# Kernel tuning notes

Hardware: AMD Instinct MI355X
Metric: run time of the kernel (lower is better)

## Reference

```python
import jax, jax.numpy as jnp
import numpy as np

N_USER, N_ITEM, N_ENT, N_REL, D = 100000, 50000, 200000, 32, 64
N_EDGE, NNZ = 500000, 2000000
N_HOPS, N_GCN, RES_LAMBDA = 2, 2, 0.5
MIN_NORM = 1e-15
BALL_EPS = 1e-3  # Poincare ball (c=1) boundary clip, standard fp32 value


def _sqnorm(x):
    return jnp.sum(x * x, axis=-1, keepdims=True)


def _norm(x):
    return jnp.maximum(jnp.sqrt(_sqnorm(x)), MIN_NORM)


def project(x):
    # clip points to the open unit ball
    n = _norm(x)
    maxn = 1.0 - BALL_EPS
    return jnp.where(n > maxn, x / n * maxn, x)


def expmap0(u):
    # exp map at origin, c=1: tanh(||u||) * u/||u||
    n = _norm(u)
    return jnp.tanh(n) * u / n


def mobius_add(x, y):
    x2, y2 = _sqnorm(x), _sqnorm(y)
    xy = jnp.sum(x * y, axis=-1, keepdims=True)
    num = (1.0 + 2.0 * xy + y2) * x + (1.0 - x2) * y
    den = 1.0 + 2.0 * xy + x2 * y2
    return num / jnp.maximum(den, MIN_NORM)


def expmap(u, p):
    # exp map at base point p of tangent vector u
    n = _norm(u)
    lam = 2.0 / jnp.maximum(1.0 - _sqnorm(p), MIN_NORM)
    return mobius_add(p, jnp.tanh(0.5 * lam * n) * u / n)


def logmap(x, p):
    # log map at base point p of point x
    sub = mobius_add(-p, x)
    n = _norm(sub)
    lam = 2.0 / jnp.maximum(1.0 - _sqnorm(p), MIN_NORM)
    return (2.0 / lam) * jnp.arctanh(jnp.minimum(n, 1.0 - 1e-5)) * sub / n


def l2norm(x):
    # F.normalize(x, dim=-1), eps=1e-12
    return x / jnp.maximum(jnp.linalg.norm(x, axis=-1, keepdims=True), 1e-12)


def rgat_agg(ent, rel, head, tail, rtype):
    he, te, re = ent[head], ent[tail], rel[rtype]  # [E, D] gathers
    ricci = l2norm(te + re)
    hh = expmap0(he)
    ht = expmap(te, hh)
    hr = expmap(re, hh)
    res = project(mobius_add(ht, hr))
    res = logmap(res, hh) + ricci * 1e-7
    res = jax.nn.relu(res)
    sums = jax.ops.segment_sum(res, head, num_segments=N_ENT)
    cnt = jax.ops.segment_sum(jnp.ones((head.shape[0], 1), res.dtype), head, num_segments=N_ENT)
    return sums / jnp.maximum(cnt, 1.0)  # scatter_mean


def setup_inputs() -> dict:
    key = jax.random.key(0)
    ks = jax.random.split(key, 9)
    return {
        "uEmbeds": jax.random.normal(ks[0], (N_USER, D), jnp.float32) * 0.02,
        "eEmbeds": jax.random.normal(ks[1], (N_ENT, D), jnp.float32) * 0.02,
        "rEmbeds": jax.random.normal(ks[2], (N_REL, D), jnp.float32) * 0.02,
        "adj_val": jax.random.uniform(ks[8], (NNZ,), jnp.float32),
        "edge_head": jax.random.randint(ks[3], (N_EDGE,), 0, N_ENT),
        "edge_tail": jax.random.randint(ks[4], (N_EDGE,), 0, N_ENT),
        "edge_type": jax.random.randint(ks[5], (N_EDGE,), 1, N_REL),
        "adj_row": jax.random.randint(ks[6], (NNZ,), 0, N_USER + N_ITEM),
        "adj_col": jax.random.randint(ks[7], (NNZ,), 0, N_USER + N_ITEM),
    }


def reference(uEmbeds, eEmbeds, rEmbeds, adj_val, edge_head, edge_tail, edge_type, adj_row, adj_col):
    rtype = edge_type - 1
    ent_res = eEmbeds
    ent = eEmbeds
    for _ in range(N_HOPS):  # RGAT hops (mess_dropout=False for determinism)
        ent = rgat_agg(ent, rEmbeds, edge_head, edge_tail, rtype)
        ent = l2norm(ent)
        ent_res = RES_LAMBDA * ent_res + ent
    # concat users with first n_items entity embeddings
    embeds = jnp.concatenate([uEmbeds, ent_res[:N_ITEM]], axis=0)  # [user+item, D]
    total = embeds
    cur = embeds
    for _ in range(N_GCN):  # GCN layers: spmm(adj, embeds) in COO form
        cur = jax.ops.segment_sum(adj_val[:, None] * cur[adj_col], adj_row,
                                  num_segments=N_USER + N_ITEM)
        total = total + cur
    # original returns (total[:N_USER], total[N_USER:]); we return the concat
    return total
```

## Files before the change

### kernel.cpp

```cpp
#include <hip/hip_runtime.h>
#include <math.h>

#define D 64
#define MIN_NORM 1e-15f
#define NBINS 64
#define MAXBKT 1024
#define L1_TILE 4096
#define WCAP_A 3840
#define WCAP_E 1024

#define RCP(x)  __builtin_amdgcn_rcpf(x)
#define RSQ(x)  __builtin_amdgcn_rsqf(x)

template <int CTRL>
__device__ __forceinline__ float dpp_sum_step(float v) {
    int iv = __builtin_bit_cast(int, v);
    int sh = __builtin_amdgcn_update_dpp(0, iv, CTRL, 0xf, 0xf, true);
    return v + __builtin_bit_cast(float, sh);
}
#define DPP_XOR1  0xB1
#define DPP_XOR2  0x4E
#define DPP_HMIR  0x141
#define DPP_MIR   0x140

__device__ __forceinline__ float row16_sum(float v) {
    v = dpp_sum_step<DPP_XOR1>(v);
    v = dpp_sum_step<DPP_XOR2>(v);
    v = dpp_sum_step<DPP_HMIR>(v);
    v = dpp_sum_step<DPP_MIR>(v);
    return v;
}


__device__ __forceinline__ float fast_tanh_pos(float x) {
    float t = __expf(-2.0f * x);
    return (1.0f - t) * RCP(1.0f + t);
}

__device__ __forceinline__ float fast_atanh(float x) {
    return 0.5f * __logf((1.0f + x) * RCP(1.0f - x));
}


__global__ void rel_prep_kernel(const float* __restrict__ rel,
                                float* __restrict__ rtab, int n_rel)
{
    int r = threadIdx.x;
    if (r >= n_rel) return;
    float s = 0.0f;
    for (int d = 0; d < D; ++d) { float v = rel[r * D + d]; s += v * v; }
    float re2g = fmaxf(s, 1e-30f);
    float rn  = RSQ(re2g);
    float nre = re2g * rn;
    float a   = fast_tanh_pos(1.0f);
    float rm2 = RCP(fmaxf(1.0f - a * a, MIN_NORM));
    rtab[r]       = s;
    rtab[64 + r]  = rn;
    rtab[128 + r] = nre;
    rtab[192 + r] = fast_tanh_pos(nre * rm2) * rn;
}


template <int HOP>
__global__ __launch_bounds__(256) void rgat_head_kernel(
    const float* __restrict__ ent, const float* __restrict__ rel,
    const int* __restrict__ erow_ptr, const int2* __restrict__ pair_e,
    const int* __restrict__ headperm,
    const float* __restrict__ prev_res,
    const float* __restrict__ rtab, float* __restrict__ te2tab,
    float* __restrict__ ent_out, float* __restrict__ res_out,
    int n_ent)
{
    int g = blockIdx.x * 16 + (threadIdx.x >> 4);
    if (g >= n_ent) return;
    int sub = threadIdx.x & 15;
    int h = headperm[g];

    const float* hp = ent + (size_t)h * D + sub;
    float hex = hp[0], hey = hp[16], hez = hp[32], hew = hp[48];

    float HE2, a, HH2, mterm, rmterm, bconst;
    if (HOP == 1) {
        HE2 = row16_sum(hex*hex + hey*hey + hez*hez + hew*hew);
        float HE2g = fmaxf(HE2, 1e-30f);
        float rNhe = RSQ(HE2g);
        float Nhe  = HE2g * rNhe;
        a = fast_tanh_pos(Nhe) * rNhe;
        HH2 = a * a * HE2;
        mterm = fmaxf(1.0f - HH2, MIN_NORM);
        rmterm = RCP(mterm);
        bconst = 0.0f;
    } else {
        HE2 = 1.0f;
        a = fast_tanh_pos(1.0f);
        HH2 = a * a;
        mterm = 1.0f - HH2;
        rmterm = RCP(mterm);
        bconst = fast_tanh_pos(rmterm);
    }

    float ax = 0.0f, ay = 0.0f, az = 0.0f, aw = 0.0f;
    int s = erow_ptr[h];
    int e = erow_ptr[h + 1];

    for (int i = s; i < e; ++i) {
        int2 pe = pair_e[i];
        int tcol = pe.x;
        int rr = pe.y - 1;
        const float* tp = ent + (size_t)tcol * D + sub;
        const float* rp = rel + (size_t)rr * D + sub;
        float tex = tp[0], tey = tp[16], tez = tp[32], tew = tp[48];
        float rex = rp[0], rey = rp[16], rez = rp[32], rew = rp[48];

        float HT = row16_sum(hex*tex + hey*tey + hez*tez + hew*tew);
        float HR = row16_sum(hex*rex + hey*rey + hez*rez + hew*rew);
        float TR = row16_sum(tex*rex + tey*rey + tez*rez + tew*rew);

        float TE2;
        if (HOP == 1) TE2 = row16_sum(tex*tex + tey*tey + tez*tez + tew*tew);
        else          TE2 = te2tab[tcol];

        float RE2  = rtab[rr];
        float rNre = rtab[64 + rr];

        float ricci_k = 1e-7f * RSQ(fmaxf(TE2 + 2.0f * TR + RE2, 1e-24f));

        float b, c;
        if (HOP == 1) {
            float TE2g = fmaxf(TE2, 1e-30f);
            float rNte = RSQ(TE2g);
            b = fast_tanh_pos(TE2g * rNte * rmterm) * rNte;
            c = fast_tanh_pos(rtab[128 + rr] * rmterm) * rNre;
        } else {
            b = bconst;
            c = rtab[192 + rr];
        }

        float y2t = b * b * TE2, xyt = a * b * HT;
        float A1 = 1.0f + 2.0f * xyt + y2t, B1 = 1.0f - HH2;
        float r_d1 = RCP(fmaxf(1.0f + 2.0f * xyt + HH2 * y2t, MIN_NORM));
        float p1 = A1 * a * r_d1, q1 = B1 * b * r_d1;
        float HT2 = fmaxf((A1*A1*HH2 + 2.0f*A1*B1*xyt + B1*B1*y2t) * r_d1 * r_d1, 0.0f);

        float y2r = c * c * RE2, xyr = a * c * HR;
        float A2 = 1.0f + 2.0f * xyr + y2r, B2 = 1.0f - HH2;
        float r_d2 = RCP(fmaxf(1.0f + 2.0f * xyr + HH2 * y2r, MIN_NORM));
        float p2 = A2 * a * r_d2, q2 = B2 * c * r_d2;
        float HR2 = fmaxf((A2*A2*HH2 + 2.0f*A2*B2*xyr + B2*B2*y2r) * r_d2 * r_d2, 0.0f);

        float xy3 = p1*p2*HE2 + p1*q2*HR + q1*p2*HT + q1*q2*TR;
        float A3 = 1.0f + 2.0f * xy3 + HR2, B3 = 1.0f - HT2;
        float r_d3 = RCP(fmaxf(1.0f + 2.0f * xy3 + HT2 * HR2, MIN_NORM));
        float al = (A3 * p1 + B3 * p2) * r_d3;
        float be = A3 * q1 * r_d3;
        float ga = B3 * q2 * r_d3;
        float R2 = fmaxf((A3*A3*HT2 + 2.0f*A3*B3*xy3 + B3*B3*HR2) * r_d3 * r_d3, 0.0f);

        float R2g = fmaxf(R2, 1e-30f);
        float rNr = RSQ(R2g);
        float Nr  = R2g * rNr;
        const float maxn = 1.0f - 1e-3f;
        if (Nr > maxn) {
            float sc = maxn * rNr;
            al *= sc; be *= sc; ga *= sc;
            R2 = maxn * maxn;
        }

        float dhr = a * (al * HE2 + be * HT + ga * HR);
        float xy4 = -dhr;
        float A4 = 1.0f + 2.0f * xy4 + R2, B4 = 1.0f - HH2;
        float r_d4 = RCP(fmaxf(1.0f + 2.0f * xy4 + HH2 * R2, MIN_NORM));
        float sh = (-A4 * a + B4 * al) * r_d4;
        float st = B4 * be * r_d4;
        float sr = B4 * ga * r_d4;
        float SUB2 = fmaxf((A4*A4*HH2 + 2.0f*A4*B4*xy4 + B4*B4*R2) * r_d4 * r_d4, 0.0f);

        float SUB2g = fmaxf(SUB2, 1e-30f);
        float rNsub = RSQ(SUB2g);
        float Nsub  = SUB2g * rNsub;
        float k = mterm * fast_atanh(fminf(Nsub, 1.0f - 1e-5f)) * rNsub;

        float kh = k * sh;
        float kt = k * st + ricci_k;
        float kr = k * sr + ricci_k;

        ax += fmaxf(kh*hex + kt*tex + kr*rex, 0.0f);
        ay += fmaxf(kh*hey + kt*tey + kr*rey, 0.0f);
        az += fmaxf(kh*hez + kt*tez + kr*rez, 0.0f);
        aw += fmaxf(kh*hew + kt*tew + kr*rew, 0.0f);
    }

    float rc = RCP(fmaxf((float)(e - s), 1.0f));
    float mx = ax*rc, my = ay*rc, mz = az*rc, mw = aw*rc;
    float M2 = row16_sum(mx*mx + my*my + mz*mz + mw*mw);
    float rn = RSQ(fmaxf(M2, 1e-24f));
    mx *= rn; my *= rn; mz *= rn; mw *= rn;

    if (HOP == 1) {
        float* ep = ent_out + (size_t)h * D + sub;
        ep[0] = mx; ep[16] = my; ep[32] = mz; ep[48] = mw;
        if (sub == 0) te2tab[h] = (M2 > 1e-24f) ? 1.0f : 0.0f;
    }
    const float* pp = prev_res + (size_t)h * D + sub;
    float* rp2 = res_out + (size_t)h * D + sub;
    rp2[0]  = 0.5f*pp[0]  + mx;
    rp2[16] = 0.5f*pp[16] + my;
    rp2[32] = 0.5f*pp[32] + mz;
    rp2[48] = 0.5f*pp[48] + mw;
}


__global__ __launch_bounds__(256) void deg_hist_kernel(
    const int* __restrict__ erow_ptr, int* __restrict__ dbins, int n_heads)
{
    __shared__ int lbin[NBINS];
    int tid = threadIdx.x;
    if (tid < NBINS) lbin[tid] = 0;
    __syncthreads();
    int h = blockIdx.x * 256 + tid;
    if (h < n_heads) {
        int d = min(erow_ptr[h + 1] - erow_ptr[h], NBINS - 1);
        atomicAdd(&lbin[d], 1);
    }
    __syncthreads();
    if (tid < NBINS) { int c = lbin[tid]; if (c) atomicAdd(&dbins[tid], c); }
}

__global__ void deg_scan_kernel(const int* __restrict__ dbins, int* __restrict__ bin_cursor)
{
    int tid = threadIdx.x;
    int v = dbins[tid];
    int incl = v;
#pragma unroll
    for (int off = 1; off < 64; off <<= 1) {
        int u = __shfl_up(incl, off, 64);
        if (tid >= off) incl += u;
    }
    int T = __shfl(incl, 63, 64);
    bin_cursor[tid] = T - incl;
}

__global__ __launch_bounds__(256) void deg_scatter_kernel(
    const int* __restrict__ erow_ptr, int* __restrict__ bin_cursor,
    int* __restrict__ headperm, int n_heads)
{
    __shared__ int lbin[NBINS];
    __shared__ int lbase[NBINS];
    int tid = threadIdx.x;
    if (tid < NBINS) lbin[tid] = 0;
    __syncthreads();
    int h = blockIdx.x * 256 + tid;
    int b = 0, lpos = 0;
    bool act = (h < n_heads);
    if (act) {
        b = min(erow_ptr[h + 1] - erow_ptr[h], NBINS - 1);
        lpos = atomicAdd(&lbin[b], 1);
    }
    __syncthreads();
    if (tid < NBINS) { int c = lbin[tid]; lbase[tid] = c ? atomicAdd(&bin_cursor[tid], c) : 0; }
    __syncthreads();
    if (act) headperm[lbase[b] + lpos] = h;
}


__global__ void concat_init_kernel(const float4* __restrict__ u,
                                   const float4* __restrict__ res,
                                   float4* __restrict__ bufA,
                                   int user4, int total4)
{
    int i = blockIdx.x * blockDim.x + threadIdx.x;
    if (i >= total4) return;
    float4 v = (i < user4) ? u[i] : res[i - user4];
    bufA[i] = v;
}


__global__ __launch_bounds__(256) void bucket_l1_kernel(
    const int* __restrict__ key, const int* __restrict__ col,
    const int* __restrict__ vbits,
    int* __restrict__ bktcur, int2* __restrict__ bkt,
    int n, int nbkt, int cap)
{
    __shared__ int lcnt[MAXBKT];
    __shared__ int lofs[MAXBKT];
    __shared__ int gofs[MAXBKT];
    __shared__ int lpos[MAXBKT];
    __shared__ int wsum[4];
    __shared__ int2 lent[L1_TILE];
    __shared__ unsigned short lbkt[L1_TILE];

    int tid  = threadIdx.x;
    int lane = tid & 63;
    int wave = tid >> 6;
    int base = blockIdx.x * L1_TILE;
    int cnt_total = min(n - base, L1_TILE);

    for (int b = tid; b < MAXBKT; b += 256) lcnt[b] = 0;
    __syncthreads();

#pragma unroll
    for (int k = 0; k < L1_TILE / 256; ++k) {
        int i = base + k * 256 + tid;
        if (i < n) atomicAdd(&lcnt[key[i] >> 8], 1);
    }
    __syncthreads();

    int b0 = tid * 4;
    int c0 = lcnt[b0], c1 = lcnt[b0 + 1], c2 = lcnt[b0 + 2], c3 = lcnt[b0 + 3];
    int tot = c0 + c1 + c2 + c3;
    int incl = tot;
#pragma unroll
    for (int off = 1; off < 64; off <<= 1) {
        int u = __shfl_up(incl, off, 64);
        if (lane >= off) incl += u;
    }
    if (lane == 63) wsum[wave] = incl;
    __syncthreads();
    int woff = 0;
    for (int w = 0; w < wave; ++w) woff += wsum[w];
    int excl = woff + incl - tot;
    lofs[b0]     = excl;                lpos[b0]     = excl;
    lofs[b0 + 1] = excl + c0;           lpos[b0 + 1] = excl + c0;
    lofs[b0 + 2] = excl + c0 + c1;      lpos[b0 + 2] = excl + c0 + c1;
    lofs[b0 + 3] = excl + c0 + c1 + c2; lpos[b0 + 3] = excl + c0 + c1 + c2;
    for (int b = tid; b < nbkt; b += 256) {
        int c = lcnt[b];
        gofs[b] = c ? atomicAdd(&bktcur[b], c) : 0;
    }
    __syncthreads();

#pragma unroll
    for (int k = 0; k < L1_TILE / 256; ++k) {
        int i = base + k * 256 + tid;
        if (i < n) {
            int r = key[i];
            int b = r >> 8;
            int p = atomicAdd(&lpos[b], 1);
            lent[p] = make_int2((col[i] << 8) | (r & 255), vbits[i]);
            lbkt[p] = (unsigned short)b;
        }
    }
    __syncthreads();

    for (int j = tid; j < cnt_total; j += 256) {
        int b = lbkt[j];
        int off = gofs[b] + (j - lofs[b]);
        if (off < cap) bkt[(size_t)b * cap + off] = lent[j];
    }
}

__global__ __launch_bounds__(256) void win_scan_kernel(
    const int* __restrict__ wincnt, int* __restrict__ winbase, int nwin, int cap)
{
    __shared__ int wsum[4];
    int tid = threadIdx.x, lane = tid & 63, wave = tid >> 6;
    int b = tid * 4;
    int c0 = (b + 0 < nwin) ? min(wincnt[b + 0], cap) : 0;
    int c1 = (b + 1 < nwin) ? min(wincnt[b + 1], cap) : 0;
    int c2 = (b + 2 < nwin) ? min(wincnt[b + 2], cap) : 0;
    int c3 = (b + 3 < nwin) ? min(wincnt[b + 3], cap) : 0;
    int tot = c0 + c1 + c2 + c3;
    int incl = tot;
#pragma unroll
    for (int off = 1; off < 64; off <<= 1) {
        int u = __shfl_up(incl, off, 64);
        if (lane >= off) incl += u;
    }
    if (lane == 63) wsum[wave] = incl;
    __syncthreads();
    int woff = 0;
    for (int w = 0; w < wave; ++w) woff += wsum[w];
    int excl = woff + incl - tot;
    if (b + 0 < nwin) winbase[b + 0] = excl;
    if (b + 1 < nwin) winbase[b + 1] = excl + c0;
    if (b + 2 < nwin) winbase[b + 2] = excl + c0 + c1;
    if (b + 3 < nwin) winbase[b + 3] = excl + c0 + c1 + c2;
}

__global__ __launch_bounds__(256) void place_l2b_kernel(
    const int* __restrict__ wincnt, const int* __restrict__ winbase,
    const int2* __restrict__ bkt,
    int2* __restrict__ pair, int* __restrict__ row_ptr,
    int n_keys, int nwin, int cap)
{
    __shared__ int rcnt[256];
    __shared__ int rofs[256];
    __shared__ int wsum[4];
    int w = blockIdx.x;
    int tid = threadIdx.x;
    int lane = tid & 63, wave = tid >> 6;
    int rbase = w << 8;
    int cnt = min(wincnt[w], cap);
    int base = winbase[w];
    const int2* seg = bkt + (size_t)w * cap;

    rcnt[tid] = 0;
    __syncthreads();
    for (int i = tid; i < cnt; i += 256)
        atomicAdd(&rcnt[bkt[(size_t)w * cap + i].x & 255], 1);
    __syncthreads();

    int v = rcnt[tid];
    int incl = v;
#pragma unroll
    for (int off = 1; off < 64; off <<= 1) {
        int u = __shfl_up(incl, off, 64);
        if (lane >= off) incl += u;
    }
    if (lane == 63) wsum[wave] = incl;
    __syncthreads();
    int woff = 0;
    for (int i = 0; i < wave; ++i) woff += wsum[i];
    int excl = woff + incl - v;
    rofs[tid] = excl;
    int r = rbase + tid;
    if (r < n_keys) row_ptr[r] = base + excl;
    if (w == nwin - 1 && tid == 255) row_ptr[n_keys] = base + excl + v;
    __syncthreads();

    for (int i = tid; i < cnt; i += 256) {
        int2 q = seg[i];
        int pos = base + atomicAdd(&rofs[q.x & 255], 1);
        pair[pos] = make_int2(q.x >> 8, q.y);
    }
}


__device__ __forceinline__ float spmm_row_gather(
    const int2* __restrict__ pair, const float* __restrict__ cur,
    int s, int e, int lane)
{
    int cnt = e - s;
    if (cnt <= 0) return 0.0f;
    int nv = min(cnt, 64);
    int2 q = pair[s + min(lane, nv - 1)];

    float acc0 = 0.0f, acc1 = 0.0f, acc2 = 0.0f, acc3 = 0.0f;
    float acc4 = 0.0f, acc5 = 0.0f, acc6 = 0.0f, acc7 = 0.0f;

    for (int base = 0; base < nv; base += 8) {
        int c0 = __builtin_amdgcn_readlane(q.x, base + 0);
        int c1 = __builtin_amdgcn_readlane(q.x, base + 1);
        int c2 = __builtin_amdgcn_readlane(q.x, base + 2);
        int c3 = __builtin_amdgcn_readlane(q.x, base + 3);
        int c4 = __builtin_amdgcn_readlane(q.x, base + 4);
        int c5 = __builtin_amdgcn_readlane(q.x, base + 5);
        int c6 = __builtin_amdgcn_readlane(q.x, base + 6);
        int c7 = __builtin_amdgcn_readlane(q.x, base + 7);
        float x0 = cur[(size_t)c0 * D + lane];
        float x1 = cur[(size_t)c1 * D + lane];
        float x2 = cur[(size_t)c2 * D + lane];
        float x3 = cur[(size_t)c3 * D + lane];
        float x4 = cur[(size_t)c4 * D + lane];
        float x5 = cur[(size_t)c5 * D + lane];
        float x6 = cur[(size_t)c6 * D + lane];
        float x7 = cur[(size_t)c7 * D + lane];
        float v0 = (base + 0 < nv) ? __int_as_float(__builtin_amdgcn_readlane(q.y, base + 0)) : 0.0f;
        float v1 = (base + 1 < nv) ? __int_as_float(__builtin_amdgcn_readlane(q.y, base + 1)) : 0.0f;
        float v2 = (base + 2 < nv) ? __int_as_float(__builtin_amdgcn_readlane(q.y, base + 2)) : 0.0f;
        float v3 = (base + 3 < nv) ? __int_as_float(__builtin_amdgcn_readlane(q.y, base + 3)) : 0.0f;
        float v4 = (base + 4 < nv) ? __int_as_float(__builtin_amdgcn_readlane(q.y, base + 4)) : 0.0f;
        float v5 = (base + 5 < nv) ? __int_as_float(__builtin_amdgcn_readlane(q.y, base + 5)) : 0.0f;
        float v6 = (base + 6 < nv) ? __int_as_float(__builtin_amdgcn_readlane(q.y, base + 6)) : 0.0f;
        float v7 = (base + 7 < nv) ? __int_as_float(__builtin_amdgcn_readlane(q.y, base + 7)) : 0.0f;
        acc0 = fmaf(v0, x0, acc0);
        acc1 = fmaf(v1, x1, acc1);
        acc2 = fmaf(v2, x2, acc2);
        acc3 = fmaf(v3, x3, acc3);
        acc4 = fmaf(v4, x4, acc4);
        acc5 = fmaf(v5, x5, acc5);
        acc6 = fmaf(v6, x6, acc6);
        acc7 = fmaf(v7, x7, acc7);
    }
    for (int i = s + 64; i < e; ++i) {
        int2 p = pair[i];
        acc0 = fmaf(__int_as_float(p.y), cur[(size_t)p.x * D + lane], acc0);
    }
    return ((acc0 + acc1) + (acc2 + acc3)) + ((acc4 + acc5) + (acc6 + acc7));
}

__global__ __launch_bounds__(256) void spmm_l1_kernel(
    const int* __restrict__ row_ptr, const int2* __restrict__ pair,
    const float* __restrict__ cur, float* __restrict__ nxt, int n_rows)
{
    int row = blockIdx.x * 4 + (threadIdx.x >> 6);
    if (row >= n_rows) return;
    int lane = threadIdx.x & 63;
    int s = row_ptr[row];
    int e = row_ptr[row + 1];
    float acc = spmm_row_gather(pair, cur, s, e, lane);
    nxt[(size_t)row * D + lane] = acc;
}

__global__ __launch_bounds__(256) void spmm_l2_kernel(
    const int* __restrict__ row_ptr, const int2* __restrict__ pair,
    const float* __restrict__ cur1, const float* __restrict__ embeds,
    float* __restrict__ out, int n_rows)
{
    int row = blockIdx.x * 4 + (threadIdx.x >> 6);
    if (row >= n_rows) return;
    int lane = threadIdx.x & 63;
    int s = row_ptr[row];
    int e = row_ptr[row + 1];
    float acc = spmm_row_gather(pair, cur1, s, e, lane);
    size_t idx = (size_t)row * D + lane;
    float emb = __builtin_nontemporal_load(embeds + idx);
    float c1  = cur1[idx];
    __builtin_nontemporal_store(emb + c1 + acc, out + idx);
}


extern "C" void kernel_launch(void* const* d_in, const int* in_sizes, int n_in,
                              void* d_out, int out_size, void* d_ws, size_t ws_size,
                              hipStream_t stream)
{
    const float* uE      = (const float*)d_in[0];
    const float* eE      = (const float*)d_in[1];
    const float* rE      = (const float*)d_in[2];
    const float* adj_val = (const float*)d_in[3];
    const int*   e_head  = (const int*)d_in[4];
    const int*   e_tail  = (const int*)d_in[5];
    const int*   e_type  = (const int*)d_in[6];
    const int*   a_row   = (const int*)d_in[7];
    const int*   a_col   = (const int*)d_in[8];

    const int n_user  = in_sizes[0] / D;
    const int n_ent   = in_sizes[1] / D;
    const int n_rel   = in_sizes[2] / D;
    const int nnz     = in_sizes[3];
    const int n_edges = in_sizes[4];
    const int n_rows  = out_size / D;

    float* ws = (float*)d_ws;
    const size_t entElems = (size_t)n_ent * D;
    float* ent1    = ws;
    float* ent_res = ws + entElems;
    int*   r3      = (int*)(ws + 2 * entElems);

    int2* ebkt = (int2*)ent_res;
    int2* abkt = (int2*)ent_res;

    const int nep = n_ent + 4;
    int*  erow_ptr = r3;
    int2* pair_e   = (int2*)(erow_ptr + nep);
    int*  headperm = (int*)(pair_e + n_edges);
    int*  dbins    = headperm + n_ent;
    int*  bincur   = dbins + NBINS;
    int*  ewincur  = bincur + NBINS;
    int*  ewinbase = ewincur + MAXBKT;
    float* te2tab  = (float*)(ewinbase + MAXBKT);
    float* rtab    = te2tab + n_ent;

    int*  row_ptr  = r3;
    int2* pair     = (int2*)(row_ptr + (n_rows + 4));
    int*  awincur  = (int*)(pair + nnz);
    int*  awinbase = awincur + MAXBKT;

    float* out = (float*)d_out;

    const int nbkt_e = (n_ent + 255) / 256;
    hipMemsetAsync(dbins, 0, (2 * NBINS + MAXBKT) * sizeof(int), stream);
    rel_prep_kernel<<<1, 64, 0, stream>>>(rE, rtab, n_rel);
    bucket_l1_kernel<<<(n_edges + L1_TILE - 1) / L1_TILE, 256, 0, stream>>>(
        e_head, e_tail, (const int*)e_type, ewincur, ebkt, n_edges, nbkt_e, WCAP_E);
    win_scan_kernel<<<1, 256, 0, stream>>>(ewincur, ewinbase, nbkt_e, WCAP_E);
    place_l2b_kernel<<<nbkt_e, 256, 0, stream>>>(ewincur, ewinbase, ebkt,
                                                 pair_e, erow_ptr, n_ent, nbkt_e, WCAP_E);
    deg_hist_kernel<<<(n_ent + 255) / 256, 256, 0, stream>>>(erow_ptr, dbins, n_ent);
    deg_scan_kernel<<<1, 64, 0, stream>>>(dbins, bincur);
    deg_scatter_kernel<<<(n_ent + 255) / 256, 256, 0, stream>>>(erow_ptr, bincur,
                                                                headperm, n_ent);

    const int head_blocks = (n_ent + 15) / 16;
    rgat_head_kernel<1><<<head_blocks, 256, 0, stream>>>(eE, rE, erow_ptr, pair_e,
                                                         headperm, eE, rtab, te2tab,
                                                         ent1, ent_res, n_ent);
    rgat_head_kernel<2><<<head_blocks, 256, 0, stream>>>(ent1, rE, erow_ptr, pair_e,
                                                         headperm, ent_res, rtab, te2tab,
                                                         ent1, ent_res, n_ent);

    float* bufA = ent1;
    float* bufB = ent_res;

    const int total4 = n_rows * (D / 4);
    const int user4  = n_user * (D / 4);

    concat_init_kernel<<<(total4 + 255) / 256, 256, 0, stream>>>(
        (const float4*)uE, (const float4*)ent_res, (float4*)bufA, user4, total4);

    const int nbkt_a = (n_rows + 255) / 256;
    hipMemsetAsync(awincur, 0, (size_t)MAXBKT * sizeof(int), stream);
    bucket_l1_kernel<<<(nnz + L1_TILE - 1) / L1_TILE, 256, 0, stream>>>(
        a_row, a_col, (const int*)adj_val, awincur, abkt, nnz, nbkt_a, WCAP_A);
    win_scan_kernel<<<1, 256, 0, stream>>>(awincur, awinbase, nbkt_a, WCAP_A);
    place_l2b_kernel<<<nbkt_a, 256, 0, stream>>>(awincur, awinbase, abkt,
                                                 pair, row_ptr, n_rows, nbkt_a, WCAP_A);

    const int row_blocks = (n_rows + 3) / 4;
    spmm_l1_kernel<<<row_blocks, 256, 0, stream>>>(row_ptr, pair, bufA, bufB, n_rows);
    spmm_l2_kernel<<<row_blocks, 256, 0, stream>>>(row_ptr, pair, bufB, bufA, out, n_rows);
}
```

Before: 555.9 us.

## Fuse scan and histogram kernels into producers via last-block-done counters

Removes the two hipMemsetAsync calls and four small kernels (win_scan twice, deg_hist, deg_scan). Zeroing moves into rel_prep and concat_init, the window scan runs in the last finishing block of bucket_l1, and the degree histogram and scan fold into place_l2b via an atomic done counter. The aim is to cut launch and serialization gaps between tiny kernels, at the cost of a threadfence and atomic per block and a serial tail in the last block. place_l2b also reads through the existing seg pointer instead of reindexing bkt.

```diff
diff --git a/kernel.cpp b/kernel.cpp
--- a/kernel.cpp
+++ b/kernel.cpp
@@ -42,10 +42,13 @@
 }
 
 
-__global__ void rel_prep_kernel(const float* __restrict__ rel,
-                                float* __restrict__ rtab, int n_rel)
-{
-    int r = threadIdx.x;
+__global__ __launch_bounds__(256) void rel_prep_kernel(
+    const float* __restrict__ rel, float* __restrict__ rtab,
+    int* __restrict__ zbase, int nzero, int n_rel)
+{
+    int tid = threadIdx.x;
+    for (int i = tid; i < nzero; i += 256) zbase[i] = 0;
+    int r = tid;
     if (r >= n_rel) return;
     float s = 0.0f;
     for (int d = 0; d < D; ++d) { float v = rel[r * D + d]; s += v * v; }
@@ -210,36 +213,6 @@
 }
 
 
-__global__ __launch_bounds__(256) void deg_hist_kernel(
-    const int* __restrict__ erow_ptr, int* __restrict__ dbins, int n_heads)
-{
-    __shared__ int lbin[NBINS];
-    int tid = threadIdx.x;
-    if (tid < NBINS) lbin[tid] = 0;
-    __syncthreads();
-    int h = blockIdx.x * 256 + tid;
-    if (h < n_heads) {
-        int d = min(erow_ptr[h + 1] - erow_ptr[h], NBINS - 1);
-        atomicAdd(&lbin[d], 1);
-    }
-    __syncthreads();
-    if (tid < NBINS) { int c = lbin[tid]; if (c) atomicAdd(&dbins[tid], c); }
-}
-
-__global__ void deg_scan_kernel(const int* __restrict__ dbins, int* __restrict__ bin_cursor)
-{
-    int tid = threadIdx.x;
-    int v = dbins[tid];
-    int incl = v;
-#pragma unroll
-    for (int off = 1; off < 64; off <<= 1) {
-        int u = __shfl_up(incl, off, 64);
-        if (tid >= off) incl += u;
-    }
-    int T = __shfl(incl, 63, 64);
-    bin_cursor[tid] = T - incl;
-}
-
 __global__ __launch_bounds__(256) void deg_scatter_kernel(
     const int* __restrict__ erow_ptr, int* __restrict__ bin_cursor,
     int* __restrict__ headperm, int n_heads)
@@ -266,9 +239,11 @@
 __global__ void concat_init_kernel(const float4* __restrict__ u,
                                    const float4* __restrict__ res,
                                    float4* __restrict__ bufA,
+                                   int* __restrict__ azero, int nzero,
                                    int user4, int total4)
 {
     int i = blockIdx.x * blockDim.x + threadIdx.x;
+    if (i < nzero) azero[i] = 0;
     if (i >= total4) return;
     float4 v = (i < user4) ? u[i] : res[i - user4];
     bufA[i] = v;
@@ -279,6 +254,7 @@
     const int* __restrict__ key, const int* __restrict__ col,
     const int* __restrict__ vbits,
     int* __restrict__ bktcur, int2* __restrict__ bkt,
+    int* __restrict__ done_ctr, int* __restrict__ winbase,
     int n, int nbkt, int cap)
 {
     __shared__ int lcnt[MAXBKT];
@@ -286,6 +262,7 @@
     __shared__ int gofs[MAXBKT];
     __shared__ int lpos[MAXBKT];
     __shared__ int wsum[4];
+    __shared__ int lastf;
     __shared__ int2 lent[L1_TILE];
     __shared__ unsigned short lbkt[L1_TILE];
 
@@ -347,40 +324,46 @@
         int off = gofs[b] + (j - lofs[b]);
         if (off < cap) bkt[(size_t)b * cap + off] = lent[j];
     }
-}
-
-__global__ __launch_bounds__(256) void win_scan_kernel(
-    const int* __restrict__ wincnt, int* __restrict__ winbase, int nwin, int cap)
-{
-    __shared__ int wsum[4];
-    int tid = threadIdx.x, lane = tid & 63, wave = tid >> 6;
-    int b = tid * 4;
-    int c0 = (b + 0 < nwin) ? min(wincnt[b + 0], cap) : 0;
-    int c1 = (b + 1 < nwin) ? min(wincnt[b + 1], cap) : 0;
-    int c2 = (b + 2 < nwin) ? min(wincnt[b + 2], cap) : 0;
-    int c3 = (b + 3 < nwin) ? min(wincnt[b + 3], cap) : 0;
-    int tot = c0 + c1 + c2 + c3;
-    int incl = tot;
+
+    __syncthreads();
+    if (tid == 0) {
+        __threadfence();
+        lastf = (atomicAdd(done_ctr, 1) == (int)gridDim.x - 1);
+    }
+    __syncthreads();
+    if (lastf) {
+        int sb = tid * 4;
+        int s0 = (sb + 0 < nbkt) ? min(atomicAdd(&bktcur[sb + 0], 0), cap) : 0;
+        int s1 = (sb + 1 < nbkt) ? min(atomicAdd(&bktcur[sb + 1], 0), cap) : 0;
+        int s2 = (sb + 2 < nbkt) ? min(atomicAdd(&bktcur[sb + 2], 0), cap) : 0;
+        int s3 = (sb + 3 < nbkt) ? min(atomicAdd(&bktcur[sb + 3], 0), cap) : 0;
+        int st = s0 + s1 + s2 + s3;
+        int sincl = st;
 #pragma unroll
-    for (int off = 1; off < 64; off <<= 1) {
-        int u = __shfl_up(incl, off, 64);
-        if (lane >= off) incl += u;
-    }
-    if (lane == 63) wsum[wave] = incl;
-    __syncthreads();
-    int woff = 0;
-    for (int w = 0; w < wave; ++w) woff += wsum[w];
-    int excl = woff + incl - tot;
-    if (b + 0 < nwin) winbase[b + 0] = excl;
-    if (b + 1 < nwin) winbase[b + 1] = excl + c0;
-    if (b + 2 < nwin) winbase[b + 2] = excl + c0 + c1;
-    if (b + 3 < nwin) winbase[b + 3] = excl + c0 + c1 + c2;
-}
-
+        for (int off = 1; off < 64; off <<= 1) {
+            int u = __shfl_up(sincl, off, 64);
+            if (lane >= off) sincl += u;
+        }
+        if (lane == 63) wsum[wave] = sincl;
+        __syncthreads();
+        int swoff = 0;
+        for (int w = 0; w < wave; ++w) swoff += wsum[w];
+        int sexcl = swoff + sincl - st;
+        if (sb + 0 < nbkt) winbase[sb + 0] = sexcl;
+        if (sb + 1 < nbkt) winbase[sb + 1] = sexcl + s0;
+        if (sb + 2 < nbkt) winbase[sb + 2] = sexcl + s0 + s1;
+        if (sb + 3 < nbkt) winbase[sb + 3] = sexcl + s0 + s1 + s2;
+    }
+}
+
+
+template <int DEG>
 __global__ __launch_bounds__(256) void place_l2b_kernel(
     const int* __restrict__ wincnt, const int* __restrict__ winbase,
     const int2* __restrict__ bkt,
     int2* __restrict__ pair, int* __restrict__ row_ptr,
+    int* __restrict__ dbins, int* __restrict__ bin_cursor,
+    int* __restrict__ done_ctr,
     int n_keys, int nwin, int cap)
 {
     __shared__ int rcnt[256];
@@ -397,7 +380,7 @@
     rcnt[tid] = 0;
     __syncthreads();
     for (int i = tid; i < cnt; i += 256)
-        atomicAdd(&rcnt[bkt[(size_t)w * cap + i].x & 255], 1);
+        atomicAdd(&rcnt[seg[i].x & 255], 1);
     __syncthreads();
 
     int v = rcnt[tid];
@@ -422,6 +405,33 @@
         int2 q = seg[i];
         int pos = base + atomicAdd(&rofs[q.x & 255], 1);
         pair[pos] = make_int2(q.x >> 8, q.y);
+    }
+
+    if (DEG) {
+        __shared__ int lbin[NBINS];
+        __shared__ int lastf;
+        if (tid < NBINS) lbin[tid] = 0;
+        __syncthreads();
+        if (r < n_keys) atomicAdd(&lbin[min(v, NBINS - 1)], 1);
+        __syncthreads();
+        if (tid < NBINS) { int cb = lbin[tid]; if (cb) atomicAdd(&dbins[tid], cb); }
+        __syncthreads();
+        if (tid == 0) {
+            __threadfence();
+            lastf = (atomicAdd(done_ctr, 1) == (int)gridDim.x - 1);
+        }
+        __syncthreads();
+        if (lastf && tid < 64) {
+            int dv = atomicAdd(&dbins[tid], 0);
+            int dincl = dv;
+#pragma unroll
+            for (int off = 1; off < 64; off <<= 1) {
+                int u = __shfl_up(dincl, off, 64);
+                if (tid >= off) dincl += u;
+            }
+            int T = __shfl(dincl, 63, 64);
+            bin_cursor[tid] = T - dincl;
+        }
     }
 }
 
@@ -547,27 +557,30 @@
     int*  dbins    = headperm + n_ent;
     int*  bincur   = dbins + NBINS;
     int*  ewincur  = bincur + NBINS;
-    int*  ewinbase = ewincur + MAXBKT;
+    int*  ectrs    = ewincur + MAXBKT;
+    int*  ewinbase = ectrs + 4;
     float* te2tab  = (float*)(ewinbase + MAXBKT);
     float* rtab    = te2tab + n_ent;
+    const int nzero_e = NBINS + NBINS + MAXBKT + 4;
 
     int*  row_ptr  = r3;
     int2* pair     = (int2*)(row_ptr + (n_rows + 4));
     int*  awincur  = (int*)(pair + nnz);
-    int*  awinbase = awincur + MAXBKT;
+    int*  actrs    = awincur + MAXBKT;
+    int*  awinbase = actrs + 4;
+    const int nzero_a = MAXBKT + 4;
 
     float* out = (float*)d_out;
 
     const int nbkt_e = (n_ent + 255) / 256;
-    hipMemsetAsync(dbins, 0, (2 * NBINS + MAXBKT) * sizeof(int), stream);
-    rel_prep_kernel<<<1, 64, 0, stream>>>(rE, rtab, n_rel);
+    rel_prep_kernel<<<1, 256, 0, stream>>>(rE, rtab, dbins, nzero_e, n_rel);
     bucket_l1_kernel<<<(n_edges + L1_TILE - 1) / L1_TILE, 256, 0, stream>>>(
-        e_head, e_tail, (const int*)e_type, ewincur, ebkt, n_edges, nbkt_e, WCAP_E);
-    win_scan_kernel<<<1, 256, 0, stream>>>(ewincur, ewinbase, nbkt_e, WCAP_E);
-    place_l2b_kernel<<<nbkt_e, 256, 0, stream>>>(ewincur, ewinbase, ebkt,
-                                                 pair_e, erow_ptr, n_ent, nbkt_e, WCAP_E);
-    deg_hist_kernel<<<(n_ent + 255) / 256, 256, 0, stream>>>(erow_ptr, dbins, n_ent);
-    deg_scan_kernel<<<1, 64, 0, stream>>>(dbins, bincur);
+        e_head, e_tail, (const int*)e_type, ewincur, ebkt, &ectrs[0], ewinbase,
+        n_edges, nbkt_e, WCAP_E);
+    place_l2b_kernel<1><<<nbkt_e, 256, 0, stream>>>(ewincur, ewinbase, ebkt,
+                                                    pair_e, erow_ptr,
+                                                    dbins, bincur, &ectrs[1],
+                                                    n_ent, nbkt_e, WCAP_E);
     deg_scatter_kernel<<<(n_ent + 255) / 256, 256, 0, stream>>>(erow_ptr, bincur,
                                                                 headperm, n_ent);
 
@@ -586,15 +599,17 @@
     const int user4  = n_user * (D / 4);
 
     concat_init_kernel<<<(total4 + 255) / 256, 256, 0, stream>>>(
-        (const float4*)uE, (const float4*)ent_res, (float4*)bufA, user4, total4);
+        (const float4*)uE, (const float4*)ent_res, (float4*)bufA,
+        awincur, nzero_a, user4, total4);
 
     const int nbkt_a = (n_rows + 255) / 256;
-    hipMemsetAsync(awincur, 0, (size_t)MAXBKT * sizeof(int), stream);
     bucket_l1_kernel<<<(nnz + L1_TILE - 1) / L1_TILE, 256, 0, stream>>>(
-        a_row, a_col, (const int*)adj_val, awincur, abkt, nnz, nbkt_a, WCAP_A);
-    win_scan_kernel<<<1, 256, 0, stream>>>(awincur, awinbase, nbkt_a, WCAP_A);
-    place_l2b_kernel<<<nbkt_a, 256, 0, stream>>>(awincur, awinbase, abkt,
-                                                 pair, row_ptr, n_rows, nbkt_a, WCAP_A);
+        a_row, a_col, (const int*)adj_val, awincur, abkt, &actrs[0], awinbase,
+        nnz, nbkt_a, WCAP_A);
+    place_l2b_kernel<0><<<nbkt_a, 256, 0, stream>>>(awincur, awinbase, abkt,
+                                                    pair, row_ptr,
+                                                    nullptr, nullptr, nullptr,
+                                                    n_rows, nbkt_a, WCAP_A);
 
     const int row_blocks = (n_rows + 3) / 4;
     spmm_l1_kernel<<<row_blocks, 256, 0, stream>>>(row_ptr, pair, bufA, bufB, n_rows);
```

Result: slower. 587.5 us (+5.7%).

## Fold window scan, degree sort and memsets into placement and prep kernels

Applied to the files above, without the earlier changes.

Removes the separate window-scan kernels by having each placement block sum the preceding window counts itself. The degree-bucketed head permutation becomes a per-256-row local sort inside the edge placement kernel, replacing the global histogram/scan/scatter chain. The memsets are folded into the relation-prep and concat kernels. This cuts about seven launches and their serialization, at the cost of redundant prefix sums per block and a head ordering that is only sorted within each 256-row window.

```diff
diff --git a/kernel.cpp b/kernel.cpp
--- a/kernel.cpp
+++ b/kernel.cpp
@@ -42,10 +42,13 @@
 }
 
 
-__global__ void rel_prep_kernel(const float* __restrict__ rel,
-                                float* __restrict__ rtab, int n_rel)
-{
-    int r = threadIdx.x;
+__global__ __launch_bounds__(256) void rel_prep_kernel(
+    const float* __restrict__ rel, float* __restrict__ rtab,
+    int* __restrict__ zbase, int nzero, int n_rel)
+{
+    int tid = threadIdx.x;
+    for (int i = tid; i < nzero; i += 256) zbase[i] = 0;
+    int r = tid;
     if (r >= n_rel) return;
     float s = 0.0f;
     for (int d = 0; d < D; ++d) { float v = rel[r * D + d]; s += v * v; }
@@ -210,65 +213,14 @@
 }
 
 
-__global__ __launch_bounds__(256) void deg_hist_kernel(
-    const int* __restrict__ erow_ptr, int* __restrict__ dbins, int n_heads)
-{
-    __shared__ int lbin[NBINS];
-    int tid = threadIdx.x;
-    if (tid < NBINS) lbin[tid] = 0;
-    __syncthreads();
-    int h = blockIdx.x * 256 + tid;
-    if (h < n_heads) {
-        int d = min(erow_ptr[h + 1] - erow_ptr[h], NBINS - 1);
-        atomicAdd(&lbin[d], 1);
-    }
-    __syncthreads();
-    if (tid < NBINS) { int c = lbin[tid]; if (c) atomicAdd(&dbins[tid], c); }
-}
-
-__global__ void deg_scan_kernel(const int* __restrict__ dbins, int* __restrict__ bin_cursor)
-{
-    int tid = threadIdx.x;
-    int v = dbins[tid];
-    int incl = v;
-#pragma unroll
-    for (int off = 1; off < 64; off <<= 1) {
-        int u = __shfl_up(incl, off, 64);
-        if (tid >= off) incl += u;
-    }
-    int T = __shfl(incl, 63, 64);
-    bin_cursor[tid] = T - incl;
-}
-
-__global__ __launch_bounds__(256) void deg_scatter_kernel(
-    const int* __restrict__ erow_ptr, int* __restrict__ bin_cursor,
-    int* __restrict__ headperm, int n_heads)
-{
-    __shared__ int lbin[NBINS];
-    __shared__ int lbase[NBINS];
-    int tid = threadIdx.x;
-    if (tid < NBINS) lbin[tid] = 0;
-    __syncthreads();
-    int h = blockIdx.x * 256 + tid;
-    int b = 0, lpos = 0;
-    bool act = (h < n_heads);
-    if (act) {
-        b = min(erow_ptr[h + 1] - erow_ptr[h], NBINS - 1);
-        lpos = atomicAdd(&lbin[b], 1);
-    }
-    __syncthreads();
-    if (tid < NBINS) { int c = lbin[tid]; lbase[tid] = c ? atomicAdd(&bin_cursor[tid], c) : 0; }
-    __syncthreads();
-    if (act) headperm[lbase[b] + lpos] = h;
-}
-
-
 __global__ void concat_init_kernel(const float4* __restrict__ u,
                                    const float4* __restrict__ res,
                                    float4* __restrict__ bufA,
+                                   int* __restrict__ azero, int nzero,
                                    int user4, int total4)
 {
     int i = blockIdx.x * blockDim.x + threadIdx.x;
+    if (i < nzero) azero[i] = 0;
     if (i >= total4) return;
     float4 v = (i < user4) ? u[i] : res[i - user4];
     bufA[i] = v;
@@ -349,55 +301,36 @@
     }
 }
 
-__global__ __launch_bounds__(256) void win_scan_kernel(
-    const int* __restrict__ wincnt, int* __restrict__ winbase, int nwin, int cap)
-{
-    __shared__ int wsum[4];
-    int tid = threadIdx.x, lane = tid & 63, wave = tid >> 6;
-    int b = tid * 4;
-    int c0 = (b + 0 < nwin) ? min(wincnt[b + 0], cap) : 0;
-    int c1 = (b + 1 < nwin) ? min(wincnt[b + 1], cap) : 0;
-    int c2 = (b + 2 < nwin) ? min(wincnt[b + 2], cap) : 0;
-    int c3 = (b + 3 < nwin) ? min(wincnt[b + 3], cap) : 0;
-    int tot = c0 + c1 + c2 + c3;
-    int incl = tot;
-#pragma unroll
-    for (int off = 1; off < 64; off <<= 1) {
-        int u = __shfl_up(incl, off, 64);
-        if (lane >= off) incl += u;
-    }
-    if (lane == 63) wsum[wave] = incl;
-    __syncthreads();
-    int woff = 0;
-    for (int w = 0; w < wave; ++w) woff += wsum[w];
-    int excl = woff + incl - tot;
-    if (b + 0 < nwin) winbase[b + 0] = excl;
-    if (b + 1 < nwin) winbase[b + 1] = excl + c0;
-    if (b + 2 < nwin) winbase[b + 2] = excl + c0 + c1;
-    if (b + 3 < nwin) winbase[b + 3] = excl + c0 + c1 + c2;
-}
-
+
+template <int PERM>
 __global__ __launch_bounds__(256) void place_l2b_kernel(
-    const int* __restrict__ wincnt, const int* __restrict__ winbase,
-    const int2* __restrict__ bkt,
+    const int* __restrict__ wincnt, const int2* __restrict__ bkt,
     int2* __restrict__ pair, int* __restrict__ row_ptr,
+    int* __restrict__ headperm,
     int n_keys, int nwin, int cap)
 {
     __shared__ int rcnt[256];
     __shared__ int rofs[256];
     __shared__ int wsum[4];
+    __shared__ int bsum[4];
     int w = blockIdx.x;
     int tid = threadIdx.x;
     int lane = tid & 63, wave = tid >> 6;
     int rbase = w << 8;
     int cnt = min(wincnt[w], cap);
-    int base = winbase[w];
     const int2* seg = bkt + (size_t)w * cap;
 
+    int part = 0;
+    for (int j = tid; j < w; j += 256) part += min(wincnt[j], cap);
+#pragma unroll
+    for (int off = 1; off < 64; off <<= 1) part += __shfl_xor(part, off, 64);
+    if (lane == 0) bsum[wave] = part;
     rcnt[tid] = 0;
     __syncthreads();
+    int base = bsum[0] + bsum[1] + bsum[2] + bsum[3];
+
     for (int i = tid; i < cnt; i += 256)
-        atomicAdd(&rcnt[bkt[(size_t)w * cap + i].x & 255], 1);
+        atomicAdd(&rcnt[seg[i].x & 255], 1);
     __syncthreads();
 
     int v = rcnt[tid];
@@ -422,6 +355,31 @@
         int2 q = seg[i];
         int pos = base + atomicAdd(&rofs[q.x & 255], 1);
         pair[pos] = make_int2(q.x >> 8, q.y);
+    }
+
+    if (PERM) {
+        __shared__ int lbin[NBINS];
+        __shared__ int lbb[NBINS];
+        if (tid < NBINS) lbin[tid] = 0;
+        __syncthreads();
+        bool act = (r < n_keys);
+        int db = min(v, NBINS - 1);
+        int lp = 0;
+        if (act) lp = atomicAdd(&lbin[db], 1);
+        __syncthreads();
+        if (tid < 64) {
+            int rb = 63 - tid;
+            int cv = lbin[rb];
+            int binc = cv;
+#pragma unroll
+            for (int off = 1; off < 64; off <<= 1) {
+                int u = __shfl_up(binc, off, 64);
+                if (tid >= off) binc += u;
+            }
+            lbb[rb] = binc - cv;
+        }
+        __syncthreads();
+        if (act) headperm[rbase + lbb[db] + lp] = r;
     }
 }
 
@@ -544,32 +502,22 @@
     int*  erow_ptr = r3;
     int2* pair_e   = (int2*)(erow_ptr + nep);
     int*  headperm = (int*)(pair_e + n_edges);
-    int*  dbins    = headperm + n_ent;
-    int*  bincur   = dbins + NBINS;
-    int*  ewincur  = bincur + NBINS;
-    int*  ewinbase = ewincur + MAXBKT;
-    float* te2tab  = (float*)(ewinbase + MAXBKT);
+    int*  ewincur  = headperm + n_ent;
+    float* te2tab  = (float*)(ewincur + MAXBKT);
     float* rtab    = te2tab + n_ent;
 
     int*  row_ptr  = r3;
     int2* pair     = (int2*)(row_ptr + (n_rows + 4));
     int*  awincur  = (int*)(pair + nnz);
-    int*  awinbase = awincur + MAXBKT;
 
     float* out = (float*)d_out;
 
     const int nbkt_e = (n_ent + 255) / 256;
-    hipMemsetAsync(dbins, 0, (2 * NBINS + MAXBKT) * sizeof(int), stream);
-    rel_prep_kernel<<<1, 64, 0, stream>>>(rE, rtab, n_rel);
+    rel_prep_kernel<<<1, 256, 0, stream>>>(rE, rtab, ewincur, MAXBKT, n_rel);
     bucket_l1_kernel<<<(n_edges + L1_TILE - 1) / L1_TILE, 256, 0, stream>>>(
         e_head, e_tail, (const int*)e_type, ewincur, ebkt, n_edges, nbkt_e, WCAP_E);
-    win_scan_kernel<<<1, 256, 0, stream>>>(ewincur, ewinbase, nbkt_e, WCAP_E);
-    place_l2b_kernel<<<nbkt_e, 256, 0, stream>>>(ewincur, ewinbase, ebkt,
-                                                 pair_e, erow_ptr, n_ent, nbkt_e, WCAP_E);
-    deg_hist_kernel<<<(n_ent + 255) / 256, 256, 0, stream>>>(erow_ptr, dbins, n_ent);
-    deg_scan_kernel<<<1, 64, 0, stream>>>(dbins, bincur);
-    deg_scatter_kernel<<<(n_ent + 255) / 256, 256, 0, stream>>>(erow_ptr, bincur,
-                                                                headperm, n_ent);
+    place_l2b_kernel<1><<<nbkt_e, 256, 0, stream>>>(ewincur, ebkt, pair_e, erow_ptr,
+                                                    headperm, n_ent, nbkt_e, WCAP_E);
 
     const int head_blocks = (n_ent + 15) / 16;
     rgat_head_kernel<1><<<head_blocks, 256, 0, stream>>>(eE, rE, erow_ptr, pair_e,
@@ -586,15 +534,14 @@
     const int user4  = n_user * (D / 4);
 
     concat_init_kernel<<<(total4 + 255) / 256, 256, 0, stream>>>(
-        (const float4*)uE, (const float4*)ent_res, (float4*)bufA, user4, total4);
+        (const float4*)uE, (const float4*)ent_res, (float4*)bufA,
+        awincur, MAXBKT, user4, total4);
 
     const int nbkt_a = (n_rows + 255) / 256;
-    hipMemsetAsync(awincur, 0, (size_t)MAXBKT * sizeof(int), stream);
     bucket_l1_kernel<<<(nnz + L1_TILE - 1) / L1_TILE, 256, 0, stream>>>(
         a_row, a_col, (const int*)adj_val, awincur, abkt, nnz, nbkt_a, WCAP_A);
-    win_scan_kernel<<<1, 256, 0, stream>>>(awincur, awinbase, nbkt_a, WCAP_A);
-    place_l2b_kernel<<<nbkt_a, 256, 0, stream>>>(awincur, awinbase, abkt,
-                                                 pair, row_ptr, n_rows, nbkt_a, WCAP_A);
+    place_l2b_kernel<0><<<nbkt_a, 256, 0, stream>>>(awincur, abkt, pair, row_ptr,
+                                                    nullptr, n_rows, nbkt_a, WCAP_A);
 
     const int row_blocks = (n_rows + 3) / 4;
     spmm_l1_kernel<<<row_blocks, 256, 0, stream>>>(row_ptr, pair, bufA, bufB, n_rows);
```

After: 662.9 us. 19.2% more time.
